# Kernel optimization log

Hardware: AMD Instinct MI355X
Metric: run time of the kernel (lower is better)

The kernel has to match this reference:

```python
import jax, jax.numpy as jnp
import numpy as np

B = 2048
INPUT_SIZE = 40960
HIDDEN = 256
ACTIVE = 30  # ~active features per chess position


def _multi_hot(key):
    idx = jax.random.randint(key, (B, ACTIVE), 0, INPUT_SIZE)
    oh = jnp.zeros((B, INPUT_SIZE), jnp.float32)
    return oh.at[jnp.arange(B)[:, None], idx].set(1.0)


def setup_inputs() -> dict:
    key = jax.random.key(0)
    kw, kb, ks, k1, k2, k3, k4 = jax.random.split(key, 7)
    white_onehot = _multi_hot(kw)
    black_onehot = _multi_hot(kb)
    stm = jax.random.randint(ks, (B, 1), 0, 2).astype(jnp.float32)
    # parameters (PyTorch Linear layout: weight [out, in])
    ft_w = jax.random.normal(k1, (HIDDEN, INPUT_SIZE), jnp.float32) * 0.02
    ft_b = jnp.zeros((HIDDEN,), jnp.float32)
    l1_w = jax.random.normal(k2, (32, HIDDEN * 2), jnp.float32) * 0.05
    l1_b = jnp.zeros((32,), jnp.float32)
    l2_w = jax.random.normal(k3, (32, 32), jnp.float32) * 0.1
    l2_b = jnp.zeros((32,), jnp.float32)
    l3_w = jax.random.normal(k4, (1, 32), jnp.float32) * 0.1
    l3_b = jnp.zeros((1,), jnp.float32)
    return dict(white_onehot=white_onehot, black_onehot=black_onehot, stm=stm,
                ft_w=ft_w, ft_b=ft_b, l1_w=l1_w, l1_b=l1_b,
                l2_w=l2_w, l2_b=l2_b, l3_w=l3_w, l3_b=l3_b)


def reference(white_onehot, black_onehot, stm,
              ft_w, ft_b, l1_w, l1_b, l2_w, l2_b, l3_w, l3_b):
    # feature transformer applied to dense one-hots (the wasteful dense GEMM)
    wh = jnp.clip(white_onehot @ ft_w.T + ft_b, 0.0, 1.0)  # [B, H]
    bh = jnp.clip(black_onehot @ ft_w.T + ft_b, 0.0, 1.0)  # [B, H]
    # side-to-move dependent perspective ordering
    hidden = jnp.where(stm.astype(bool),
                       jnp.concatenate([wh, bh], axis=-1),
                       jnp.concatenate([bh, wh], axis=-1))  # [B, 2H]
    x = jnp.clip(hidden @ l1_w.T + l1_b, 0.0, 1.0)
    x = jnp.clip(x @ l2_w.T + l2_b, 0.0, 1.0)
    return x @ l3_w.T + l3_b  # [B, 1]
```

## Files before the change

### kernel.cpp

```cpp
#include <hip/hip_runtime.h>

#define BATCH 2048
#define IN_SZ 40960
#define IN4   (IN_SZ / 4)
#define HID   256
#define LCAP  64

__global__ __launch_bounds__(256) void ft_transpose(const float* __restrict__ ftw,
                                                    float* __restrict__ ftT) {
    __shared__ float tile[32][33];
    const int tx = threadIdx.x;
    const int ty = threadIdx.y;
    const int bx = blockIdx.x;
    const int by = blockIdx.y;

    const int col = bx * 32 + tx;
#pragma unroll
    for (int j = 0; j < 32; j += 8) {
        const int row = by * 32 + ty + j;
        tile[ty + j][tx] = ftw[(size_t)row * IN_SZ + col];
    }
    __syncthreads();

    const int ocol = by * 32 + tx;
#pragma unroll
    for (int j = 0; j < 32; j += 8) {
        const int orow = bx * 32 + ty + j;
        ftT[(size_t)orow * HID + ocol] = tile[tx][ty + j];
    }
}

__global__ __launch_bounds__(256) void nnue_fused(
    const float* __restrict__ wo, const float* __restrict__ bo,
    const float* __restrict__ stm,
    const float* __restrict__ ftT,
    const float* __restrict__ ftb,
    const float* __restrict__ l1w, const float* __restrict__ l1b,
    const float* __restrict__ l2w, const float* __restrict__ l2b,
    const float* __restrict__ l3w, const float* __restrict__ l3b,
    float* __restrict__ out) {
    __shared__ int   idxw[LCAP], idxb[LCAP];
    __shared__ int   cntw, cntb;
    __shared__ float hidden[2 * HID];
    __shared__ float x1[32], x2[32];

    const int b = blockIdx.x;
    const int t = threadIdx.x;

    if (t == 0) { cntw = 0; cntb = 0; }
    __syncthreads();

    {
        const uint4* __restrict__ wrow = (const uint4*)(wo + (size_t)b * IN_SZ);
        const uint4* __restrict__ brow = (const uint4*)(bo + (size_t)b * IN_SZ);
#pragma unroll 1
        for (int i0 = t; i0 < IN4; i0 += 512) {
            const int i1 = i0 + 256;
            const uint4 w0 = wrow[i0];
            const uint4 w1 = wrow[i1];
            const uint4 b0 = brow[i0];
            const uint4 b1 = brow[i1];
            const unsigned mw0 = w0.x | w0.y | w0.z | w0.w;
            const unsigned mw1 = w1.x | w1.y | w1.z | w1.w;
            const unsigned mb0 = b0.x | b0.y | b0.z | b0.w;
            const unsigned mb1 = b1.x | b1.y | b1.z | b1.w;
            if (__any(mw0 | mw1)) {
                if (w0.x) idxw[atomicAdd(&cntw, 1)] = 4 * i0;
                if (w0.y) idxw[atomicAdd(&cntw, 1)] = 4 * i0 + 1;
                if (w0.z) idxw[atomicAdd(&cntw, 1)] = 4 * i0 + 2;
                if (w0.w) idxw[atomicAdd(&cntw, 1)] = 4 * i0 + 3;
                if (w1.x) idxw[atomicAdd(&cntw, 1)] = 4 * i1;
                if (w1.y) idxw[atomicAdd(&cntw, 1)] = 4 * i1 + 1;
                if (w1.z) idxw[atomicAdd(&cntw, 1)] = 4 * i1 + 2;
                if (w1.w) idxw[atomicAdd(&cntw, 1)] = 4 * i1 + 3;
            }
            if (__any(mb0 | mb1)) {
                if (b0.x) idxb[atomicAdd(&cntb, 1)] = 4 * i0;
                if (b0.y) idxb[atomicAdd(&cntb, 1)] = 4 * i0 + 1;
                if (b0.z) idxb[atomicAdd(&cntb, 1)] = 4 * i0 + 2;
                if (b0.w) idxb[atomicAdd(&cntb, 1)] = 4 * i0 + 3;
                if (b1.x) idxb[atomicAdd(&cntb, 1)] = 4 * i1;
                if (b1.y) idxb[atomicAdd(&cntb, 1)] = 4 * i1 + 1;
                if (b1.z) idxb[atomicAdd(&cntb, 1)] = 4 * i1 + 2;
                if (b1.w) idxb[atomicAdd(&cntb, 1)] = 4 * i1 + 3;
            }
        }
    }
    __syncthreads();

    const int cw = cntw, cb = cntb;
    float accw = ftb[t];
    float accb = accw;
    for (int j = 0; j < cw; ++j) accw += ftT[(size_t)idxw[j] * HID + t];
    for (int j = 0; j < cb; ++j) accb += ftT[(size_t)idxb[j] * HID + t];
    accw = fminf(fmaxf(accw, 0.f), 1.f);
    accb = fminf(fmaxf(accb, 0.f), 1.f);

    const bool s = (stm[b] != 0.f);
    hidden[t]       = s ? accw : accb;
    hidden[HID + t] = s ? accb : accw;
    __syncthreads();

    {
        const int o = t >> 3;
        const int part = t & 7;
        const float* w1p = l1w + o * (2 * HID);
        float sum = 0.f;
#pragma unroll 8
        for (int i = part; i < 2 * HID; i += 8)
            sum += hidden[i] * w1p[i];
        sum += __shfl_xor(sum, 1);
        sum += __shfl_xor(sum, 2);
        sum += __shfl_xor(sum, 4);
        if (part == 0) x1[o] = fminf(fmaxf(sum + l1b[o], 0.f), 1.f);
    }
    __syncthreads();

    if (t < 32) {
        const float* w2 = l2w + t * 32;
        float sum = l2b[t];
#pragma unroll
        for (int i = 0; i < 32; ++i) sum += x1[i] * w2[i];
        x2[t] = fminf(fmaxf(sum, 0.f), 1.f);
    }
    __syncthreads();

    if (t == 0) {
        float sum = l3b[0];
#pragma unroll
        for (int i = 0; i < 32; ++i) sum += x2[i] * l3w[i];
        out[b] = sum;
    }
}

__global__ __launch_bounds__(256) void nnue_fused_fallback(
    const float* __restrict__ wo, const float* __restrict__ bo,
    const float* __restrict__ stm,
    const float* __restrict__ ftw, const float* __restrict__ ftb,
    const float* __restrict__ l1w, const float* __restrict__ l1b,
    const float* __restrict__ l2w, const float* __restrict__ l2b,
    const float* __restrict__ l3w, const float* __restrict__ l3b,
    float* __restrict__ out) {
    __shared__ int   idxw[LCAP], idxb[LCAP];
    __shared__ int   cntw, cntb;
    __shared__ float hidden[2 * HID];
    __shared__ float x1[32], x2[32];

    const int b = blockIdx.x;
    const int t = threadIdx.x;
    if (t == 0) { cntw = 0; cntb = 0; }
    __syncthreads();

    const uint4* wrow = (const uint4*)(wo + (size_t)b * IN_SZ);
    const uint4* brow = (const uint4*)(bo + (size_t)b * IN_SZ);
    for (int i = t; i < IN4; i += 256) {
        uint4 v = wrow[i];
        uint4 u = brow[i];
        if (v.x | v.y | v.z | v.w) {
            if (v.x) idxw[atomicAdd(&cntw, 1)] = 4 * i;
            if (v.y) idxw[atomicAdd(&cntw, 1)] = 4 * i + 1;
            if (v.z) idxw[atomicAdd(&cntw, 1)] = 4 * i + 2;
            if (v.w) idxw[atomicAdd(&cntw, 1)] = 4 * i + 3;
        }
        if (u.x | u.y | u.z | u.w) {
            if (u.x) idxb[atomicAdd(&cntb, 1)] = 4 * i;
            if (u.y) idxb[atomicAdd(&cntb, 1)] = 4 * i + 1;
            if (u.z) idxb[atomicAdd(&cntb, 1)] = 4 * i + 2;
            if (u.w) idxb[atomicAdd(&cntb, 1)] = 4 * i + 3;
        }
    }
    __syncthreads();

    float accw = ftb[t], accb = accw;
    for (int j = 0; j < cntw; ++j) accw += ftw[(size_t)t * IN_SZ + idxw[j]];
    for (int j = 0; j < cntb; ++j) accb += ftw[(size_t)t * IN_SZ + idxb[j]];
    accw = fminf(fmaxf(accw, 0.f), 1.f);
    accb = fminf(fmaxf(accb, 0.f), 1.f);

    const bool s = (stm[b] != 0.f);
    hidden[t]       = s ? accw : accb;
    hidden[HID + t] = s ? accb : accw;
    __syncthreads();

    {
        const int o = t >> 3, part = t & 7;
        const float* w1p = l1w + o * (2 * HID);
        float sum = 0.f;
        for (int i = part; i < 2 * HID; i += 8) sum += hidden[i] * w1p[i];
        sum += __shfl_xor(sum, 1);
        sum += __shfl_xor(sum, 2);
        sum += __shfl_xor(sum, 4);
        if (part == 0) x1[o] = fminf(fmaxf(sum + l1b[o], 0.f), 1.f);
    }
    __syncthreads();
    if (t < 32) {
        float sum = l2b[t];
        for (int i = 0; i < 32; ++i) sum += x1[i] * l2w[t * 32 + i];
        x2[t] = fminf(fmaxf(sum, 0.f), 1.f);
    }
    __syncthreads();
    if (t == 0) {
        float sum = l3b[0];
        for (int i = 0; i < 32; ++i) sum += x2[i] * l3w[i];
        out[b] = sum;
    }
}

extern "C" void kernel_launch(void* const* d_in, const int* in_sizes, int n_in,
                              void* d_out, int out_size, void* d_ws, size_t ws_size,
                              hipStream_t stream) {
    const float* wo  = (const float*)d_in[0];
    const float* bo  = (const float*)d_in[1];
    const float* stm = (const float*)d_in[2];
    const float* ftw = (const float*)d_in[3];
    const float* ftb = (const float*)d_in[4];
    const float* l1w = (const float*)d_in[5];
    const float* l1b = (const float*)d_in[6];
    const float* l2w = (const float*)d_in[7];
    const float* l2b = (const float*)d_in[8];
    const float* l3w = (const float*)d_in[9];
    const float* l3b = (const float*)d_in[10];
    float* out = (float*)d_out;

    const size_t ftT_bytes = (size_t)IN_SZ * HID * sizeof(float);
    if (ws_size >= ftT_bytes) {
        float* ftT = (float*)d_ws;
        ft_transpose<<<dim3(IN_SZ / 32, HID / 32), dim3(32, 8), 0, stream>>>(ftw, ftT);
        nnue_fused<<<BATCH, 256, 0, stream>>>(wo, bo, stm, ftT, ftb,
                                              l1w, l1b, l2w, l2b, l3w, l3b, out);
    } else {
        nnue_fused_fallback<<<BATCH, 256, 0, stream>>>(wo, bo, stm, ftw, ftb,
                                                       l1w, l1b, l2w, l2b, l3w, l3b, out);
    }
}
```

Measured before the change: 691.8 us.

## Overlap weight transpose with sparse index scan in one launch, then gather+MLP

Merges the feature-weight transpose and the per-row nonzero scan into a single launch whose blocks split between the two jobs, so both memory-bound passes run concurrently. Scanned index lists and counts go to global workspace, and a second kernel gathers the transposed weights and runs the MLP. The scan also issues four vector loads per operand per iteration instead of two and drops the wave-level any-skip. The cost is an extra global round trip for the lists and a larger workspace requirement, which falls back to the slow path if not met.

```diff
diff --git a/kernel.cpp b/kernel.cpp
--- a/kernel.cpp
+++ b/kernel.cpp
@@ -5,94 +5,105 @@
 #define IN4   (IN_SZ / 4)
 #define HID   256
 #define LCAP  64
-
-__global__ __launch_bounds__(256) void ft_transpose(const float* __restrict__ ftw,
-                                                    float* __restrict__ ftT) {
-    __shared__ float tile[32][33];
-    const int tx = threadIdx.x;
-    const int ty = threadIdx.y;
-    const int bx = blockIdx.x;
-    const int by = blockIdx.y;
-
-    const int col = bx * 32 + tx;
-#pragma unroll
-    for (int j = 0; j < 32; j += 8) {
-        const int row = by * 32 + ty + j;
-        tile[ty + j][tx] = ftw[(size_t)row * IN_SZ + col];
-    }
-    __syncthreads();
-
-    const int ocol = by * 32 + tx;
-#pragma unroll
-    for (int j = 0; j < 32; j += 8) {
-        const int orow = bx * 32 + ty + j;
-        ftT[(size_t)orow * HID + ocol] = tile[tx][ty + j];
-    }
-}
-
-__global__ __launch_bounds__(256) void nnue_fused(
+#define TBLK  1280
+#define NBA   (TBLK + BATCH)
+
+#define FTT_OFF   0
+#define CNT_OFF   (44u * 1024u * 1024u)
+#define LIST_OFF  (CNT_OFF + BATCH * 2 * sizeof(int))
+
+__global__ __launch_bounds__(256) void prep_scan(
     const float* __restrict__ wo, const float* __restrict__ bo,
+    const float* __restrict__ ftw,
+    float* __restrict__ ftT,
+    int* __restrict__ cntg,
+    int* __restrict__ listg)
+{
+    const int t = threadIdx.x;
+
+    if (blockIdx.x < TBLK) {
+        __shared__ float tile[32][33];
+        const int bx = blockIdx.x;
+        const int tx = t & 31;
+        const int ty = t >> 5;
+        for (int by = 0; by < 8; ++by) {
+            __syncthreads();
+#pragma unroll
+            for (int j = 0; j < 32; j += 8)
+                tile[ty + j][tx] = ftw[(size_t)(by * 32 + ty + j) * IN_SZ + bx * 32 + tx];
+            __syncthreads();
+#pragma unroll
+            for (int j = 0; j < 32; j += 8)
+                ftT[(size_t)(bx * 32 + ty + j) * HID + by * 32 + tx] = tile[tx][ty + j];
+        }
+        return;
+    }
+
+    __shared__ int idxw[LCAP], idxb[LCAP];
+    __shared__ int cntw, cntb;
+    const int row = blockIdx.x - TBLK;
+    if (t == 0) { cntw = 0; cntb = 0; }
+    __syncthreads();
+
+    const uint4* __restrict__ wrow = (const uint4*)(wo + (size_t)row * IN_SZ);
+    const uint4* __restrict__ brow = (const uint4*)(bo + (size_t)row * IN_SZ);
+#pragma unroll 1
+    for (int base = t; base < IN4; base += 1024) {
+        uint4 W[4], Bv[4];
+#pragma unroll
+        for (int k = 0; k < 4; ++k) W[k]  = wrow[base + k * 256];
+#pragma unroll
+        for (int k = 0; k < 4; ++k) Bv[k] = brow[base + k * 256];
+#pragma unroll
+        for (int k = 0; k < 4; ++k) {
+            const int f0 = 4 * (base + k * 256);
+            if (W[k].x) idxw[atomicAdd(&cntw, 1)] = f0;
+            if (W[k].y) idxw[atomicAdd(&cntw, 1)] = f0 + 1;
+            if (W[k].z) idxw[atomicAdd(&cntw, 1)] = f0 + 2;
+            if (W[k].w) idxw[atomicAdd(&cntw, 1)] = f0 + 3;
+        }
+#pragma unroll
+        for (int k = 0; k < 4; ++k) {
+            const int f0 = 4 * (base + k * 256);
+            if (Bv[k].x) idxb[atomicAdd(&cntb, 1)] = f0;
+            if (Bv[k].y) idxb[atomicAdd(&cntb, 1)] = f0 + 1;
+            if (Bv[k].z) idxb[atomicAdd(&cntb, 1)] = f0 + 2;
+            if (Bv[k].w) idxb[atomicAdd(&cntb, 1)] = f0 + 3;
+        }
+    }
+    __syncthreads();
+
+    if (t == 0) { cntg[row * 2] = cntw; cntg[row * 2 + 1] = cntb; }
+    if (t < cntw) listg[(row * 2) * LCAP + t] = idxw[t];
+    if (t < cntb) listg[(row * 2 + 1) * LCAP + t] = idxb[t];
+}
+
+__global__ __launch_bounds__(256) void gather_mlp(
+    const int* __restrict__ cntg, const int* __restrict__ listg,
     const float* __restrict__ stm,
-    const float* __restrict__ ftT,
-    const float* __restrict__ ftb,
+    const float* __restrict__ ftT, const float* __restrict__ ftb,
     const float* __restrict__ l1w, const float* __restrict__ l1b,
     const float* __restrict__ l2w, const float* __restrict__ l2b,
     const float* __restrict__ l3w, const float* __restrict__ l3b,
-    float* __restrict__ out) {
-    __shared__ int   idxw[LCAP], idxb[LCAP];
-    __shared__ int   cntw, cntb;
+    float* __restrict__ out)
+{
+    __shared__ int   sidx[2 * LCAP];
     __shared__ float hidden[2 * HID];
     __shared__ float x1[32], x2[32];
 
     const int b = blockIdx.x;
     const int t = threadIdx.x;
 
-    if (t == 0) { cntw = 0; cntb = 0; }
-    __syncthreads();
-
-    {
-        const uint4* __restrict__ wrow = (const uint4*)(wo + (size_t)b * IN_SZ);
-        const uint4* __restrict__ brow = (const uint4*)(bo + (size_t)b * IN_SZ);
-#pragma unroll 1
-        for (int i0 = t; i0 < IN4; i0 += 512) {
-            const int i1 = i0 + 256;
-            const uint4 w0 = wrow[i0];
-            const uint4 w1 = wrow[i1];
-            const uint4 b0 = brow[i0];
-            const uint4 b1 = brow[i1];
-            const unsigned mw0 = w0.x | w0.y | w0.z | w0.w;
-            const unsigned mw1 = w1.x | w1.y | w1.z | w1.w;
-            const unsigned mb0 = b0.x | b0.y | b0.z | b0.w;
-            const unsigned mb1 = b1.x | b1.y | b1.z | b1.w;
-            if (__any(mw0 | mw1)) {
-                if (w0.x) idxw[atomicAdd(&cntw, 1)] = 4 * i0;
-                if (w0.y) idxw[atomicAdd(&cntw, 1)] = 4 * i0 + 1;
-                if (w0.z) idxw[atomicAdd(&cntw, 1)] = 4 * i0 + 2;
-                if (w0.w) idxw[atomicAdd(&cntw, 1)] = 4 * i0 + 3;
-                if (w1.x) idxw[atomicAdd(&cntw, 1)] = 4 * i1;
-                if (w1.y) idxw[atomicAdd(&cntw, 1)] = 4 * i1 + 1;
-                if (w1.z) idxw[atomicAdd(&cntw, 1)] = 4 * i1 + 2;
-                if (w1.w) idxw[atomicAdd(&cntw, 1)] = 4 * i1 + 3;
-            }
-            if (__any(mb0 | mb1)) {
-                if (b0.x) idxb[atomicAdd(&cntb, 1)] = 4 * i0;
-                if (b0.y) idxb[atomicAdd(&cntb, 1)] = 4 * i0 + 1;
-                if (b0.z) idxb[atomicAdd(&cntb, 1)] = 4 * i0 + 2;
-                if (b0.w) idxb[atomicAdd(&cntb, 1)] = 4 * i0 + 3;
-                if (b1.x) idxb[atomicAdd(&cntb, 1)] = 4 * i1;
-                if (b1.y) idxb[atomicAdd(&cntb, 1)] = 4 * i1 + 1;
-                if (b1.z) idxb[atomicAdd(&cntb, 1)] = 4 * i1 + 2;
-                if (b1.w) idxb[atomicAdd(&cntb, 1)] = 4 * i1 + 3;
-            }
-        }
-    }
-    __syncthreads();
-
-    const int cw = cntw, cb = cntb;
+    if (t < 2 * LCAP) sidx[t] = listg[b * 2 * LCAP + t];
+    __syncthreads();
+
+    const int cw = cntg[b * 2 + 0];
+    const int cb = cntg[b * 2 + 1];
+
     float accw = ftb[t];
     float accb = accw;
-    for (int j = 0; j < cw; ++j) accw += ftT[(size_t)idxw[j] * HID + t];
-    for (int j = 0; j < cb; ++j) accb += ftT[(size_t)idxb[j] * HID + t];
+    for (int j = 0; j < cw; ++j) accw += ftT[(size_t)sidx[j] * HID + t];
+    for (int j = 0; j < cb; ++j) accb += ftT[(size_t)sidx[LCAP + j] * HID + t];
     accw = fminf(fmaxf(accw, 0.f), 1.f);
     accb = fminf(fmaxf(accb, 0.f), 1.f);
 
@@ -222,11 +233,14 @@
     const float* l3b = (const float*)d_in[10];
     float* out = (float*)d_out;
 
-    const size_t ftT_bytes = (size_t)IN_SZ * HID * sizeof(float);
-    if (ws_size >= ftT_bytes) {
-        float* ftT = (float*)d_ws;
-        ft_transpose<<<dim3(IN_SZ / 32, HID / 32), dim3(32, 8), 0, stream>>>(ftw, ftT);
-        nnue_fused<<<BATCH, 256, 0, stream>>>(wo, bo, stm, ftT, ftb,
+    const size_t need = LIST_OFF + (size_t)BATCH * 2 * LCAP * sizeof(int);
+    if (ws_size >= need) {
+        float* ftT  = (float*)((char*)d_ws + FTT_OFF);
+        int* cntg   = (int*)((char*)d_ws + CNT_OFF);
+        int* listg  = (int*)((char*)d_ws + LIST_OFF);
+
+        prep_scan<<<NBA, 256, 0, stream>>>(wo, bo, ftw, ftT, cntg, listg);
+        gather_mlp<<<BATCH, 256, 0, stream>>>(cntg, listg, stm, ftT, ftb,
                                               l1w, l1b, l2w, l2b, l3w, l3b, out);
     } else {
         nnue_fused_fallback<<<BATCH, 256, 0, stream>>>(wo, bo, stm, ftw, ftb,
```

Result: no change. 695.3 us (+0.5%).
